# Performance work log

Measured on AMD Instinct MI355X. Metric: run time of the kernel, lower is better.

## Reference

```python
import jax, jax.numpy as jnp
import numpy as np

NUM_SPLITS = 2  # attn_splits


def _split_c_last(x, ns):
    # split_feature(channel_last=True): [b,h,w,c] -> [b*ns*ns, h/ns, w/ns, c]
    b, h, w, c = x.shape
    x = x.reshape(b, ns, h // ns, ns, w // ns, c)
    x = jnp.transpose(x, (0, 1, 3, 2, 4, 5))
    return x.reshape(b * ns * ns, h // ns, w // ns, c)


def _merge_c_last(x, ns):
    # merge_splits(channel_last=True): [b*ns*ns, hh, ww, c] -> [b, ns*hh, ns*ww, c]
    bn, hh, ww, c = x.shape
    b = bn // (ns * ns)
    x = x.reshape(b, ns, ns, hh, ww, c)
    x = jnp.transpose(x, (0, 1, 3, 2, 4, 5))
    return x.reshape(b, ns * hh, ns * ww, c)


def _make_shift_window_mask(h, w, ns):
    # exact port of generate_shift_window_attn_mask (numpy, setup-time only)
    wh, ww = h // ns, w // ns
    sh, sw = wh // 2, ww // 2
    img = np.zeros((h, w))
    cnt = 0
    for hs in (slice(0, -wh), slice(-wh, -sh), slice(-sh, None)):
        for ws in (slice(0, -ww), slice(-ww, -sw), slice(-sw, None)):
            img[hs, ws] = cnt
            cnt += 1
    mw = img.reshape(ns, wh, ns, ww).transpose(0, 2, 1, 3).reshape(ns * ns, wh * ww)
    am = mw[:, None, :] - mw[:, :, None]  # [n, i, j] = mw[n, j] - mw[n, i]
    am = np.where(am != 0, -100.0, 0.0).astype(np.float32)
    return jnp.asarray(am)


def _window_attention(q, k, v, attn_mask, h, w, ns):
    # single_head_split_window_attention with with_shift=True
    b, hw, c = q.shape
    sh, sw = (h // ns) // 2, (w // ns) // 2

    def prep(x):
        x = x.reshape(b, h, w, c)
        x = jnp.roll(x, shift=(-sh, -sw), axis=(1, 2))
        return _split_c_last(x, ns).reshape(b * ns * ns, -1, c)

    qs, ks, vs = prep(q), prep(k), prep(v)
    scale = jnp.asarray(c, q.dtype) ** 0.5
    scores = jnp.einsum('bqc,bkc->bqk', qs, ks) / scale
    scores = scores + jnp.tile(attn_mask, (b, 1, 1))
    attn = jax.nn.softmax(scores, axis=-1)
    out = jnp.einsum('bqk,bkc->bqc', attn, vs)
    out = _merge_c_last(out.reshape(b * ns * ns, h // ns, w // ns, c), ns)
    out = jnp.roll(out, shift=(sh, sw), axis=(1, 2))
    return out.reshape(b, hw, c)


def _global_correlation_softmax(feature0, feature1):
    b, c, h, w = feature0.shape
    hw = h * w
    f0 = feature0.reshape(b, c, hw).transpose(0, 2, 1)  # [b, hw, c]
    f1 = feature1.reshape(b, c, hw)                     # [b, c, hw]
    scale = jnp.asarray(c, feature0.dtype) ** 0.5
    corr = jnp.matmul(f0, f1) / scale                   # [b, hw, hw]

    yy, xx = jnp.meshgrid(jnp.arange(h), jnp.arange(w), indexing='ij')
    init_grid = jnp.stack([xx, yy], axis=0).astype(feature0.dtype)  # [2,h,w]
    init_grid = jnp.broadcast_to(init_grid[None], (b, 2, h, w))
    grid = init_grid.reshape(b, 2, hw).transpose(0, 2, 1)            # [b, hw, 2]

    corr2 = jnp.concatenate([corr, jnp.transpose(corr, (0, 2, 1))], axis=0)  # [2b,hw,hw]
    grid2 = jnp.tile(grid, (2, 1, 1))
    init2 = jnp.tile(init_grid, (2, 1, 1, 1))

    prob = jax.nn.softmax(corr2, axis=-1)
    corresp = jnp.matmul(prob, grid2).reshape(2 * b, h, w, 2)
    corresp = jnp.transpose(corresp, (0, 3, 1, 2))
    flow = corresp - init2
    f01, f10 = flow[:b], flow[b:]
    dual_prob = prob[:b] * jnp.transpose(prob[b:], (0, 2, 1))
    return f01, f10, dual_prob


def setup_inputs() -> dict:
    key = jax.random.key(0)
    b, c, h, w = 2, 128, 48, 96
    ks = jax.random.split(key, 5)
    q = jax.random.normal(ks[0], (b, h * w, c), dtype=jnp.float32)
    k = jax.random.normal(ks[1], (b, h * w, c), dtype=jnp.float32)
    v = jax.random.normal(ks[2], (b, h * w, c), dtype=jnp.float32)
    feature0 = jax.random.normal(ks[3], (b, c, h, w), dtype=jnp.float32)
    feature1 = jax.random.normal(ks[4], (b, c, h, w), dtype=jnp.float32)
    attn_mask = _make_shift_window_mask(h, w, NUM_SPLITS)
    return {"q": q, "k": k, "v": v, "feature0": feature0, "feature1": feature1,
            "attn_mask": attn_mask, "h": h, "w": w}


def reference(q, k, v, feature0, feature1, attn_mask, h, w):
    attn_out = _window_attention(q, k, v, attn_mask, h, w, NUM_SPLITS)
    f01, f10, dual_prob = _global_correlation_softmax(feature0, feature1)
    return (attn_out, f01, f10, dual_prob)
```

## Files before the change

### kernel.cpp

```cpp
#include <hip/hip_runtime.h>

#define HW 4608
#define CC 128
#define H 48
#define W 96
#define S_WIN 1152
#define SCALE 0.08838834764831845f

typedef __attribute__((ext_vector_type(8))) short bf16x8;
typedef __attribute__((ext_vector_type(4))) float f32x4;

static __device__ inline short f2bf(float f) {
    unsigned u = __builtin_bit_cast(unsigned, f);
    unsigned r = (u + 0x7fff + ((u >> 16) & 1)) >> 16;
    return (short)r;
}

__global__ __launch_bounds__(256)
void prep_all(const float* __restrict__ Q, const float* __restrict__ K, const float* __restrict__ V,
              const float* __restrict__ f0, const float* __restrict__ f1,
              bf16x8* __restrict__ cfragA, bf16x8* __restrict__ cfragB,
              bf16x8* __restrict__ qfrag, bf16x8* __restrict__ kfrag, bf16x8* __restrict__ vfrag,
              float* __restrict__ wsf)
{
    __shared__ float vt[32][132];
    const int bx = blockIdx.x;
    const int t = threadIdx.x;

    if (bx < 1152) {
        int zi = bx * 256 + t;
        if (zi < 12 * HW) wsf[zi] = 0.f;
        const int pt = bx % 72;
        const int z  = bx / 72;
        const int tensor = z >> 3, b = (z >> 2) & 1, kc = z & 3;
        const float* src = (tensor ? f1 : f0) + (size_t)b * CC * HW + (size_t)kc * 32 * HW + pt * 64;
        {
            int ch = t >> 4;
            int c4 = (t & 15) * 4;
            *(float4*)&vt[ch][c4]      = *(const float4*)&src[(size_t)ch * HW + c4];
            *(float4*)&vt[ch + 16][c4] = *(const float4*)&src[(size_t)(ch + 16) * HW + c4];
        }
        __syncthreads();
        int Rloc = t >> 6, lane = t & 63;
        int R = pt * 4 + Rloc;
        bf16x8 v;
        #pragma unroll
        for (int j = 0; j < 8; ++j) v[j] = f2bf(vt[(lane >> 4) * 8 + j][Rloc * 16 + (lane & 15)]);
        (tensor ? cfragB : cfragA)[((size_t)(b * 288 + R) * 4 + kc) * 64 + lane] = v;
    } else {
        const int bx2 = bx - 1152;
        const int R2 = bx2 % 36;
        const int z  = bx2 / 36;
        const int tensor = z >> 3, wb = z & 7;
        const int bb = wb >> 2, wi = wb & 3, si = wi >> 1, sj = wi & 1;
        const float* src = (tensor == 0 ? Q : (tensor == 1 ? K : V)) + (size_t)bb * HW * CC;
        {
            int row = t >> 3;
            int c16 = (t & 7) * 16;
            int qw = R2 * 32 + row;
            int rr = qw / 48, cc = qw - rr * 48;
            int y = (si * 24 + rr + 12) % 48;
            int x = (sj * 48 + cc + 24) % 96;
            const float* rp = src + ((size_t)y * 96 + x) * CC + c16;
            #pragma unroll
            for (int u = 0; u < 4; ++u)
                *(float4*)&vt[row][c16 + u * 4] = *(const float4*)&rp[u * 4];
        }
        __syncthreads();
        if (tensor < 2) {
            bf16x8* frag = tensor == 0 ? qfrag : kfrag;
            #pragma unroll
            for (int e2 = 0; e2 < 2; ++e2) {
                int e = t + e2 * 256;
                int Rloc = e >> 8, kc = (e >> 6) & 3, lane = e & 63;
                int R = R2 * 2 + Rloc;
                bf16x8 v;
                #pragma unroll
                for (int j = 0; j < 8; ++j)
                    v[j] = f2bf(vt[Rloc * 16 + (lane & 15)][kc * 32 + (lane >> 4) * 8 + j]);
                frag[((size_t)(wb * 72 + R) * 4 + kc) * 64 + lane] = v;
            }
        } else {
            #pragma unroll
            for (int e2 = 0; e2 < 2; ++e2) {
                int e = t + e2 * 256;
                int dB = e >> 6, lane = e & 63;
                bf16x8 v;
                #pragma unroll
                for (int j = 0; j < 8; ++j)
                    v[j] = f2bf(vt[(lane >> 4) * 8 + j][dB * 16 + (lane & 15)]);
                vfrag[((size_t)(wb * 8 + dB) * 36 + R2) * 64 + lane] = v;
            }
        }
    }
}

__global__ __launch_bounds__(256)
void fused_ws(const bf16x8* __restrict__ qfrag, const bf16x8* __restrict__ kfrag,
              const bf16x8* __restrict__ vfrag, float* __restrict__ out,
              const bf16x8* __restrict__ cfragA, const bf16x8* __restrict__ cfragB,
              float* __restrict__ rowsum, float* __restrict__ colsum)
{
    __shared__ __align__(16) char smem[38144];
    const int bx = blockIdx.x;
    const int t = threadIdx.x, lane = t & 63, w = t >> 6;

    if (bx < 576) {
        short* Psh = (short*)smem;
        unsigned char* codes = (unsigned char*)(smem + 36864);
        float* rsum_sh = (float*)(smem + 38016);
        const int qt = bx % 72, wb = bx / 72;
        const int bb = wb >> 2, wi = wb & 3, si = wi >> 1, sj = wi & 1;

        if (t < 16) rsum_sh[t] = 0.f;
        for (int i = t; i < S_WIN; i += 256) {
            int r = i / 48, c = i - r * 48;
            codes[i] = (unsigned char)((si ? (r >= 12) : 0) | ((sj ? (c >= 24) : 0) << 1));
        }
        __syncthreads();

        bf16x8 qf[4];
        {
            const bf16x8* qb = qfrag + ((size_t)(wb * 72 + qt) * 4) * 64 + lane;
            #pragma unroll
            for (int kc = 0; kc < 4; ++kc) qf[kc] = qb[kc * 64];
        }
        const int qcode = codes[qt * 16 + (lane & 15)];
        char* Pb = (char*)Psh;
        float rsum = 0.f;

        for (int kt = 0; kt < 18; ++kt) {
            int Rk = w * 18 + kt;
            const bf16x8* kb = kfrag + ((size_t)(wb * 72 + Rk) * 4) * 64 + lane;
            bf16x8 kf[4];
            #pragma unroll
            for (int kc = 0; kc < 4; ++kc) kf[kc] = kb[kc * 64];
            int k0 = Rk * 16 + (lane >> 4) * 4;
            f32x4 acc = {0.f, 0.f, 0.f, 0.f};
            #pragma unroll
            for (int kc = 0; kc < 4; ++kc)
                acc = __builtin_amdgcn_mfma_f32_16x16x32_bf16(kf[kc], qf[kc], acc, 0, 0, 0);
            float ev[4];
            #pragma unroll
            for (int r = 0; r < 4; ++r) {
                ev[r] = (codes[k0 + r] == qcode) ? __expf(acc[r] * SCALE) : 0.f;
                rsum += ev[r];
            }
            unsigned lo = (unsigned)(unsigned short)f2bf(ev[0]) | ((unsigned)(unsigned short)f2bf(ev[1]) << 16);
            unsigned hi = (unsigned)(unsigned short)f2bf(ev[2]) | ((unsigned)(unsigned short)f2bf(ev[3]) << 16);
            int qloc = lane & 15;
            int off = (qloc * 2304 + k0 * 2) ^ ((qloc & 7) << 4);
            *(uint2*)(Pb + off) = make_uint2(lo, hi);
        }
        rsum += __shfl_xor(rsum, 16); rsum += __shfl_xor(rsum, 32);
        if (lane < 16) atomicAdd(&rsum_sh[lane], rsum);
        __syncthreads();

        f32x4 pv0 = {0.f, 0.f, 0.f, 0.f}, pv1 = {0.f, 0.f, 0.f, 0.f};
        const bf16x8* vb0 = vfrag + ((size_t)(wb * 8 + w) * 36) * 64 + lane;
        const bf16x8* vb1 = vfrag + ((size_t)(wb * 8 + w + 4) * 36) * 64 + lane;
        for (int kc = 0; kc < 36; ++kc) {
            int qloc = lane & 15;
            int off = (qloc * 2304 + kc * 64 + (lane >> 4) * 16) ^ ((qloc & 7) << 4);
            bf16x8 pf = *(const bf16x8*)(Pb + off);
            pv0 = __builtin_amdgcn_mfma_f32_16x16x32_bf16(pf, vb0[kc * 64], pv0, 0, 0, 0);
            pv1 = __builtin_amdgcn_mfma_f32_16x16x32_bf16(pf, vb1[kc * 64], pv1, 0, 0, 0);
        }
        #pragma unroll
        for (int r = 0; r < 4; ++r) {
            int qloc = (lane >> 4) * 4 + r;
            float rinv = 1.f / rsum_sh[qloc];
            int qw = qt * 16 + qloc;
            int rr = qw / 48, cc2 = qw - rr * 48;
            int y = (si * 24 + rr + 12) % 48;
            int x = (sj * 48 + cc2 + 24) % 96;
            float* op = &out[((size_t)bb * HW + y * 96 + x) * CC + (lane & 15)];
            op[w * 16]       = pv0[r] * rinv;
            op[(w + 4) * 16] = pv1[r] * rinv;
        }
    } else {
        float* rs = (float*)smem;
        float* cs = (float*)(smem + 512);
        const int bx2 = bx - 576;
        const int kt = bx2 % 36, qt = (bx2 / 36) % 36, b = bx2 / 1296;
        const int wm = w >> 1, wn = w & 1;

        const bf16x8* Ab = cfragA + (size_t)(b * 288 + qt * 8 + wm * 4) * 256 + lane;
        const bf16x8* Bb = cfragB + (size_t)(b * 288 + kt * 8 + wn * 4) * 256 + lane;

        f32x4 acc[4][4] = {};
        #pragma unroll
        for (int kc = 0; kc < 4; ++kc) {
            bf16x8 a[4], bf[4];
            #pragma unroll
            for (int m = 0; m < 4; ++m) a[m]  = Ab[(m * 4 + kc) * 64];
            #pragma unroll
            for (int n = 0; n < 4; ++n) bf[n] = Bb[(n * 4 + kc) * 64];
            #pragma unroll
            for (int m = 0; m < 4; ++m)
                #pragma unroll
                for (int n = 0; n < 4; ++n)
                    acc[m][n] = __builtin_amdgcn_mfma_f32_16x16x32_bf16(a[m], bf[n], acc[m][n], 0, 0, 0);
        }

        if (t < 128) { rs[t] = 0.f; cs[t] = 0.f; }
        __syncthreads();

        float cv[4] = {};
        #pragma unroll
        for (int m = 0; m < 4; ++m) {
            float rv[4] = {};
            #pragma unroll
            for (int n = 0; n < 4; ++n)
                #pragma unroll
                for (int r = 0; r < 4; ++r) {
                    float ev = __expf(acc[m][n][r] * SCALE);
                    rv[r] += ev; cv[n] += ev;
                }
            #pragma unroll
            for (int r = 0; r < 4; ++r) {
                float s = rv[r];
                s += __shfl_xor(s, 1); s += __shfl_xor(s, 2);
                s += __shfl_xor(s, 4); s += __shfl_xor(s, 8);
                if ((lane & 15) == 0)
                    atomicAdd(&rs[wm * 64 + m * 16 + (lane >> 4) * 4 + r], s);
            }
        }
        #pragma unroll
        for (int n = 0; n < 4; ++n) {
            float s = cv[n];
            s += __shfl_xor(s, 16); s += __shfl_xor(s, 32);
            if (lane < 16) atomicAdd(&cs[wn * 64 + n * 16 + lane], s);
        }
        __syncthreads();
        if (t < 128)      atomicAdd(&rowsum[(size_t)b * HW + qt * 128 + t], rs[t]);
        else              atomicAdd(&colsum[(size_t)b * HW + kt * 128 + (t - 128)], cs[t - 128]);
    }
}

__global__ __launch_bounds__(256)
void corr_final(const bf16x8* __restrict__ fragA, const bf16x8* __restrict__ fragB,
                const float* __restrict__ rowsum, const float* __restrict__ colsum,
                float* __restrict__ rowflow, float* __restrict__ colflow,
                float* __restrict__ dual)
{
    __shared__ float sfx[128], sfy[128], scx[128], scy[128];
    __shared__ float stg[4][16][68];
    const int t = threadIdx.x, lane = t & 63, wave = t >> 6;
    const int wm = wave >> 1, wn = wave & 1;
    const int kt = blockIdx.x, qt = blockIdx.y, b = blockIdx.z;

    const bf16x8* Ab = fragA + (size_t)(b * 288 + qt * 8 + wm * 4) * 256 + lane;
    const bf16x8* Bb = fragB + (size_t)(b * 288 + kt * 8 + wn * 4) * 256 + lane;

    f32x4 acc[4][4] = {};
    #pragma unroll
    for (int kc = 0; kc < 4; ++kc) {
        bf16x8 a[4], bf[4];
        #pragma unroll
        for (int m = 0; m < 4; ++m) a[m]  = Ab[(m * 4 + kc) * 64];
        #pragma unroll
        for (int n = 0; n < 4; ++n) bf[n] = Bb[(n * 4 + kc) * 64];
        #pragma unroll
        for (int m = 0; m < 4; ++m)
            #pragma unroll
            for (int n = 0; n < 4; ++n)
                acc[m][n] = __builtin_amdgcn_mfma_f32_16x16x32_bf16(a[m], bf[n], acc[m][n], 0, 0, 0);
    }

    if (t < 128) { sfx[t] = 0.f; sfy[t] = 0.f; scx[t] = 0.f; scy[t] = 0.f; }
    __syncthreads();

    const int qbase = qt * 128 + wm * 64;
    const int kbase = kt * 128 + wn * 64;

    float cinv[4], gkx[4], gky[4];
    #pragma unroll
    for (int n = 0; n < 4; ++n) {
        int k = kbase + n * 16 + (lane & 15);
        cinv[n] = 1.f / colsum[(size_t)b * HW + k];
        int kyi = k / W;
        gkx[n] = (float)(k - kyi * W); gky[n] = (float)kyi;
    }

    float cfx[4] = {}, cfy[4] = {};
    #pragma unroll
    for (int m = 0; m < 4; ++m) {
        float rinv[4], gqx[4], gqy[4];
        int q0 = qbase + m * 16 + (lane >> 4) * 4;
        #pragma unroll
        for (int r = 0; r < 4; ++r) {
            rinv[r] = 1.f / rowsum[(size_t)b * HW + q0 + r];
            int qyi = (q0 + r) / W;
            gqx[r] = (float)(q0 + r - qyi * W); gqy[r] = (float)qyi;
        }
        float rfx[4] = {}, rfy[4] = {};
        #pragma unroll
        for (int n = 0; n < 4; ++n) {
            #pragma unroll
            for (int r = 0; r < 4; ++r) {
                float ev = __expf(acc[m][n][r] * SCALE);
                float rp = ev * rinv[r];
                float ce = ev * cinv[n];
                stg[wave][(lane >> 4) * 4 + r][n * 16 + (lane & 15)] = rp * ce;
                rfx[r] += rp * gkx[n]; rfy[r] += rp * gky[n];
                cfx[n] += ce * gqx[r]; cfy[n] += ce * gqy[r];
            }
        }
        #pragma unroll
        for (int pass = 0; pass < 4; ++pass) {
            int row = pass * 4 + (lane >> 4);
            f32x4 vv = *(const f32x4*)&stg[wave][row][(lane & 15) * 4];
            __builtin_nontemporal_store(vv,
                (f32x4*)&dual[((size_t)b * HW + qbase + m * 16 + row) * HW + kbase + (lane & 15) * 4]);
        }
        #pragma unroll
        for (int r = 0; r < 4; ++r) {
            float sx = rfx[r], sy = rfy[r];
            sx += __shfl_xor(sx, 1); sx += __shfl_xor(sx, 2);
            sx += __shfl_xor(sx, 4); sx += __shfl_xor(sx, 8);
            sy += __shfl_xor(sy, 1); sy += __shfl_xor(sy, 2);
            sy += __shfl_xor(sy, 4); sy += __shfl_xor(sy, 8);
            if ((lane & 15) == 0) {
                int row = wm * 64 + m * 16 + (lane >> 4) * 4 + r;
                atomicAdd(&sfx[row], sx); atomicAdd(&sfy[row], sy);
            }
        }
    }
    #pragma unroll
    for (int n = 0; n < 4; ++n) {
        float sx = cfx[n], sy = cfy[n];
        sx += __shfl_xor(sx, 16); sx += __shfl_xor(sx, 32);
        sy += __shfl_xor(sy, 16); sy += __shfl_xor(sy, 32);
        if (lane < 16) {
            int col = wn * 64 + n * 16 + lane;
            atomicAdd(&scx[col], sx); atomicAdd(&scy[col], sy);
        }
    }
    __syncthreads();
    if (t < 128) {
        atomicAdd(&rowflow[((size_t)b * HW + qt * 128 + t) * 2 + 0], sfx[t]);
        atomicAdd(&rowflow[((size_t)b * HW + qt * 128 + t) * 2 + 1], sfy[t]);
    } else {
        int j = t - 128;
        atomicAdd(&colflow[((size_t)b * HW + kt * 128 + j) * 2 + 0], scx[j]);
        atomicAdd(&colflow[((size_t)b * HW + kt * 128 + j) * 2 + 1], scy[j]);
    }
}

__global__ void flow_finalize(const float* __restrict__ rowflow, const float* __restrict__ colflow,
                              float* __restrict__ out)
{
    int i = blockIdx.x * 256 + threadIdx.x;
    if (i >= 2 * 2 * HW) return;
    int bb   = i / (2 * HW);
    int rem  = i % (2 * HW);
    int chan = rem / HW;
    int q    = rem % HW;
    float g = (chan == 0) ? (float)(q % W) : (float)(q / W);
    out[i]              = rowflow[((size_t)bb * HW + q) * 2 + chan] - g;
    out[2 * 2 * HW + i] = colflow[((size_t)bb * HW + q) * 2 + chan] - g;
}

extern "C" void kernel_launch(void* const* d_in, const int* in_sizes, int n_in,
                              void* d_out, int out_size, void* d_ws, size_t ws_size,
                              hipStream_t stream)
{
    (void)in_sizes; (void)n_in; (void)out_size; (void)ws_size;
    const float* q  = (const float*)d_in[0];
    const float* k  = (const float*)d_in[1];
    const float* v  = (const float*)d_in[2];
    const float* f0 = (const float*)d_in[3];
    const float* f1 = (const float*)d_in[4];

    float* out = (float*)d_out;
    const size_t ATTN_SZ = (size_t)2 * HW * CC;
    const size_t FLOW_SZ = (size_t)2 * 2 * HW;
    float* f01  = out + ATTN_SZ;
    float* dual = out + ATTN_SZ + 2 * FLOW_SZ;

    const size_t FR = 2359296;
    char* wsb = (char*)d_ws;
    bf16x8* cfragA = (bf16x8*)(wsb);
    bf16x8* cfragB = (bf16x8*)(wsb + FR);
    bf16x8* qfrag  = (bf16x8*)(wsb + 2 * FR);
    bf16x8* kfrag  = (bf16x8*)(wsb + 3 * FR);
    bf16x8* vfrag  = (bf16x8*)(wsb + 4 * FR);
    float* wsf     = (float*)(wsb + 5 * FR);
    float* rowsum  = wsf;
    float* colsum  = wsf + 2 * HW;
    float* rowflow = wsf + 4 * HW;
    float* colflow = wsf + 8 * HW;

    prep_all<<<dim3(2016), 256, 0, stream>>>(q, k, v, f0, f1, cfragA, cfragB,
                                             qfrag, kfrag, vfrag, wsf);
    fused_ws<<<dim3(576 + 2592), 256, 0, stream>>>(qfrag, kfrag, vfrag, out,
                                                   cfragA, cfragB, rowsum, colsum);
    corr_final<<<dim3(36, 36, 2), 256, 0, stream>>>(cfragA, cfragB, rowsum, colsum,
                                                    rowflow, colflow, dual);
    flow_finalize<<<dim3(72), 256, 0, stream>>>(rowflow, colflow, f01);
}
```

Before: 113.7 us.

## Split window attention P buffer into two key chunks to halve LDS

The window-attention branch now processes the 1152 keys in two chunks of 576. Each chunk writes its P tile to shared memory, then PV MFMAs consume it, which halves the P buffer and shrinks total LDS from about 38KB to about 19.7KB. The goal is more resident blocks per CU and better latency hiding. The cost is an extra barrier pair per chunk, and the correlation branch of the same kernel must now fit in the smaller shared allocation.

```diff
diff --git a/kernel.cpp b/kernel.cpp
--- a/kernel.cpp
+++ b/kernel.cpp
@@ -101,14 +101,14 @@
               const bf16x8* __restrict__ cfragA, const bf16x8* __restrict__ cfragB,
               float* __restrict__ rowsum, float* __restrict__ colsum)
 {
-    __shared__ __align__(16) char smem[38144];
+    __shared__ __align__(16) char smem[19712];
     const int bx = blockIdx.x;
     const int t = threadIdx.x, lane = t & 63, w = t >> 6;
 
     if (bx < 576) {
-        short* Psh = (short*)smem;
-        unsigned char* codes = (unsigned char*)(smem + 36864);
-        float* rsum_sh = (float*)(smem + 38016);
+        char* Pb = smem;
+        unsigned char* codes = (unsigned char*)(smem + 18432);
+        float* rsum_sh = (float*)(smem + 19584);
         const int qt = bx % 72, wb = bx / 72;
         const int bb = wb >> 2, wi = wb & 3, si = wi >> 1, sj = wi & 1;
 
@@ -126,51 +126,58 @@
             for (int kc = 0; kc < 4; ++kc) qf[kc] = qb[kc * 64];
         }
         const int qcode = codes[qt * 16 + (lane & 15)];
-        char* Pb = (char*)Psh;
+        const int qloc = lane & 15;
         float rsum = 0.f;
-
-        for (int kt = 0; kt < 18; ++kt) {
-            int Rk = w * 18 + kt;
-            const bf16x8* kb = kfrag + ((size_t)(wb * 72 + Rk) * 4) * 64 + lane;
-            bf16x8 kf[4];
-            #pragma unroll
-            for (int kc = 0; kc < 4; ++kc) kf[kc] = kb[kc * 64];
-            int k0 = Rk * 16 + (lane >> 4) * 4;
-            f32x4 acc = {0.f, 0.f, 0.f, 0.f};
-            #pragma unroll
-            for (int kc = 0; kc < 4; ++kc)
-                acc = __builtin_amdgcn_mfma_f32_16x16x32_bf16(kf[kc], qf[kc], acc, 0, 0, 0);
-            float ev[4];
-            #pragma unroll
-            for (int r = 0; r < 4; ++r) {
-                ev[r] = (codes[k0 + r] == qcode) ? __expf(acc[r] * SCALE) : 0.f;
-                rsum += ev[r];
-            }
-            unsigned lo = (unsigned)(unsigned short)f2bf(ev[0]) | ((unsigned)(unsigned short)f2bf(ev[1]) << 16);
-            unsigned hi = (unsigned)(unsigned short)f2bf(ev[2]) | ((unsigned)(unsigned short)f2bf(ev[3]) << 16);
-            int qloc = lane & 15;
-            int off = (qloc * 2304 + k0 * 2) ^ ((qloc & 7) << 4);
-            *(uint2*)(Pb + off) = make_uint2(lo, hi);
-        }
-        rsum += __shfl_xor(rsum, 16); rsum += __shfl_xor(rsum, 32);
-        if (lane < 16) atomicAdd(&rsum_sh[lane], rsum);
-        __syncthreads();
-
         f32x4 pv0 = {0.f, 0.f, 0.f, 0.f}, pv1 = {0.f, 0.f, 0.f, 0.f};
         const bf16x8* vb0 = vfrag + ((size_t)(wb * 8 + w) * 36) * 64 + lane;
         const bf16x8* vb1 = vfrag + ((size_t)(wb * 8 + w + 4) * 36) * 64 + lane;
-        for (int kc = 0; kc < 36; ++kc) {
-            int qloc = lane & 15;
-            int off = (qloc * 2304 + kc * 64 + (lane >> 4) * 16) ^ ((qloc & 7) << 4);
-            bf16x8 pf = *(const bf16x8*)(Pb + off);
-            pv0 = __builtin_amdgcn_mfma_f32_16x16x32_bf16(pf, vb0[kc * 64], pv0, 0, 0, 0);
-            pv1 = __builtin_amdgcn_mfma_f32_16x16x32_bf16(pf, vb1[kc * 64], pv1, 0, 0, 0);
+
+        #pragma unroll
+        for (int chunk = 0; chunk < 2; ++chunk) {
+            for (int kt = 0; kt < 9; ++kt) {
+                int Rk = chunk * 36 + w * 9 + kt;
+                const bf16x8* kb = kfrag + ((size_t)(wb * 72 + Rk) * 4) * 64 + lane;
+                bf16x8 kf[4];
+                #pragma unroll
+                for (int kc = 0; kc < 4; ++kc) kf[kc] = kb[kc * 64];
+                int k0 = Rk * 16 + (lane >> 4) * 4;
+                f32x4 acc = {0.f, 0.f, 0.f, 0.f};
+                #pragma unroll
+                for (int kc = 0; kc < 4; ++kc)
+                    acc = __builtin_amdgcn_mfma_f32_16x16x32_bf16(kf[kc], qf[kc], acc, 0, 0, 0);
+                float ev[4];
+                #pragma unroll
+                for (int r = 0; r < 4; ++r) {
+                    ev[r] = (codes[k0 + r] == qcode) ? __expf(acc[r] * SCALE) : 0.f;
+                    rsum += ev[r];
+                }
+                unsigned lo = (unsigned)(unsigned short)f2bf(ev[0]) | ((unsigned)(unsigned short)f2bf(ev[1]) << 16);
+                unsigned hi = (unsigned)(unsigned short)f2bf(ev[2]) | ((unsigned)(unsigned short)f2bf(ev[3]) << 16);
+                int klocal = k0 - chunk * 576;
+                int off = (qloc * 1152 + klocal * 2) ^ ((qloc & 7) << 4);
+                *(uint2*)(Pb + off) = make_uint2(lo, hi);
+            }
+            if (chunk == 1) {
+                float s = rsum;
+                s += __shfl_xor(s, 16); s += __shfl_xor(s, 32);
+                if (lane < 16) atomicAdd(&rsum_sh[lane], s);
+            }
+            __syncthreads();
+            #pragma unroll 2
+            for (int kcl = 0; kcl < 18; ++kcl) {
+                int kcg = chunk * 18 + kcl;
+                int off = (qloc * 1152 + kcl * 64 + (lane >> 4) * 16) ^ ((qloc & 7) << 4);
+                bf16x8 pf = *(const bf16x8*)(Pb + off);
+                pv0 = __builtin_amdgcn_mfma_f32_16x16x32_bf16(pf, vb0[kcg * 64], pv0, 0, 0, 0);
+                pv1 = __builtin_amdgcn_mfma_f32_16x16x32_bf16(pf, vb1[kcg * 64], pv1, 0, 0, 0);
+            }
+            __syncthreads();
         }
         #pragma unroll
         for (int r = 0; r < 4; ++r) {
-            int qloc = (lane >> 4) * 4 + r;
-            float rinv = 1.f / rsum_sh[qloc];
-            int qw = qt * 16 + qloc;
+            int ql = (lane >> 4) * 4 + r;
+            float rinv = 1.f / rsum_sh[ql];
+            int qw = qt * 16 + ql;
             int rr = qw / 48, cc2 = qw - rr * 48;
             int y = (si * 24 + rr + 12) % 48;
             int x = (sj * 48 + cc2 + 24) % 96;
```

New measurement: 126.7 us. 11.4% more time.

## Compute flow sums from unnormalized exp in first pass, fold finalize into dual kernel

Applied to the files above, without the earlier changes.

The row and column flow accumulations (exp weighted by grid coordinates) move into the first correlation pass alongside the row and column sums. Normalization by rowsum and colsum is applied later in a finalize step, so the second pass only writes the dual probability matrix. The separate finalize kernel is merged into the second pass as extra blocks, which removes one launch and the shuffle and atomic reduction work in the store-heavy pass. In exchange the first pass does more accumulation and atomics, and the finalize blocks depend on the previous kernel's results, which stream ordering already guarantees.

```diff
diff --git a/kernel.cpp b/kernel.cpp
--- a/kernel.cpp
+++ b/kernel.cpp
@@ -99,7 +99,8 @@
 void fused_ws(const bf16x8* __restrict__ qfrag, const bf16x8* __restrict__ kfrag,
               const bf16x8* __restrict__ vfrag, float* __restrict__ out,
               const bf16x8* __restrict__ cfragA, const bf16x8* __restrict__ cfragB,
-              float* __restrict__ rowsum, float* __restrict__ colsum)
+              float* __restrict__ rowsum, float* __restrict__ colsum,
+              float* __restrict__ rowflow, float* __restrict__ colflow)
 {
     __shared__ __align__(16) char smem[38144];
     const int bx = blockIdx.x;
@@ -179,8 +180,12 @@
             op[(w + 4) * 16] = pv1[r] * rinv;
         }
     } else {
-        float* rs = (float*)smem;
-        float* cs = (float*)(smem + 512);
+        float* rs   = (float*)smem;
+        float* rfxs = (float*)(smem + 512);
+        float* rfys = (float*)(smem + 1024);
+        float* cs   = (float*)(smem + 1536);
+        float* cfxs = (float*)(smem + 2048);
+        float* cfys = (float*)(smem + 2560);
         const int bx2 = bx - 576;
         const int kt = bx2 % 36, qt = (bx2 / 36) % 36, b = bx2 / 1296;
         const int wm = w >> 1, wn = w & 1;
@@ -203,52 +208,99 @@
                     acc[m][n] = __builtin_amdgcn_mfma_f32_16x16x32_bf16(a[m], bf[n], acc[m][n], 0, 0, 0);
         }
 
-        if (t < 128) { rs[t] = 0.f; cs[t] = 0.f; }
-        __syncthreads();
-
-        float cv[4] = {};
+        if (t < 128) { rs[t] = 0.f; rfxs[t] = 0.f; rfys[t] = 0.f; cs[t] = 0.f; cfxs[t] = 0.f; cfys[t] = 0.f; }
+        __syncthreads();
+
+        const int qbase = qt * 128 + wm * 64;
+        const int kbase = kt * 128 + wn * 64;
+        float gkx[4], gky[4];
+        #pragma unroll
+        for (int n = 0; n < 4; ++n) {
+            int k = kbase + n * 16 + (lane & 15);
+            int kyi = k / W;
+            gkx[n] = (float)(k - kyi * W); gky[n] = (float)kyi;
+        }
+
+        float cv[4] = {}, cfx[4] = {}, cfy[4] = {};
         #pragma unroll
         for (int m = 0; m < 4; ++m) {
-            float rv[4] = {};
+            float gqx[4], gqy[4];
+            int q0 = qbase + m * 16 + (lane >> 4) * 4;
+            #pragma unroll
+            for (int r = 0; r < 4; ++r) {
+                int qyi = (q0 + r) / W;
+                gqx[r] = (float)(q0 + r - qyi * W); gqy[r] = (float)qyi;
+            }
+            float rv[4] = {}, rfx[4] = {}, rfy[4] = {};
             #pragma unroll
             for (int n = 0; n < 4; ++n)
                 #pragma unroll
                 for (int r = 0; r < 4; ++r) {
                     float ev = __expf(acc[m][n][r] * SCALE);
-                    rv[r] += ev; cv[n] += ev;
+                    rv[r] += ev; rfx[r] += ev * gkx[n]; rfy[r] += ev * gky[n];
+                    cv[n] += ev; cfx[n] += ev * gqx[r]; cfy[n] += ev * gqy[r];
                 }
             #pragma unroll
             for (int r = 0; r < 4; ++r) {
-                float s = rv[r];
-                s += __shfl_xor(s, 1); s += __shfl_xor(s, 2);
-                s += __shfl_xor(s, 4); s += __shfl_xor(s, 8);
-                if ((lane & 15) == 0)
-                    atomicAdd(&rs[wm * 64 + m * 16 + (lane >> 4) * 4 + r], s);
+                float s0 = rv[r], s1 = rfx[r], s2 = rfy[r];
+                s0 += __shfl_xor(s0, 1); s0 += __shfl_xor(s0, 2); s0 += __shfl_xor(s0, 4); s0 += __shfl_xor(s0, 8);
+                s1 += __shfl_xor(s1, 1); s1 += __shfl_xor(s1, 2); s1 += __shfl_xor(s1, 4); s1 += __shfl_xor(s1, 8);
+                s2 += __shfl_xor(s2, 1); s2 += __shfl_xor(s2, 2); s2 += __shfl_xor(s2, 4); s2 += __shfl_xor(s2, 8);
+                if ((lane & 15) == 0) {
+                    int row = wm * 64 + m * 16 + (lane >> 4) * 4 + r;
+                    atomicAdd(&rs[row], s0); atomicAdd(&rfxs[row], s1); atomicAdd(&rfys[row], s2);
+                }
             }
         }
         #pragma unroll
         for (int n = 0; n < 4; ++n) {
-            float s = cv[n];
-            s += __shfl_xor(s, 16); s += __shfl_xor(s, 32);
-            if (lane < 16) atomicAdd(&cs[wn * 64 + n * 16 + lane], s);
-        }
-        __syncthreads();
-        if (t < 128)      atomicAdd(&rowsum[(size_t)b * HW + qt * 128 + t], rs[t]);
-        else              atomicAdd(&colsum[(size_t)b * HW + kt * 128 + (t - 128)], cs[t - 128]);
+            float s0 = cv[n], s1 = cfx[n], s2 = cfy[n];
+            s0 += __shfl_xor(s0, 16); s0 += __shfl_xor(s0, 32);
+            s1 += __shfl_xor(s1, 16); s1 += __shfl_xor(s1, 32);
+            s2 += __shfl_xor(s2, 16); s2 += __shfl_xor(s2, 32);
+            if (lane < 16) {
+                int col = wn * 64 + n * 16 + lane;
+                atomicAdd(&cs[col], s0); atomicAdd(&cfxs[col], s1); atomicAdd(&cfys[col], s2);
+            }
+        }
+        __syncthreads();
+        if (t < 128) {
+            atomicAdd(&rowsum[(size_t)b * HW + qt * 128 + t], rs[t]);
+            atomicAdd(&rowflow[((size_t)b * HW + qt * 128 + t) * 2 + 0], rfxs[t]);
+            atomicAdd(&rowflow[((size_t)b * HW + qt * 128 + t) * 2 + 1], rfys[t]);
+        } else {
+            int j = t - 128;
+            atomicAdd(&colsum[(size_t)b * HW + kt * 128 + j], cs[j]);
+            atomicAdd(&colflow[((size_t)b * HW + kt * 128 + j) * 2 + 0], cfxs[j]);
+            atomicAdd(&colflow[((size_t)b * HW + kt * 128 + j) * 2 + 1], cfys[j]);
+        }
     }
 }
 
 __global__ __launch_bounds__(256)
-void corr_final(const bf16x8* __restrict__ fragA, const bf16x8* __restrict__ fragB,
-                const float* __restrict__ rowsum, const float* __restrict__ colsum,
-                float* __restrict__ rowflow, float* __restrict__ colflow,
-                float* __restrict__ dual)
+void fused_final(const bf16x8* __restrict__ fragA, const bf16x8* __restrict__ fragB,
+                 const float* __restrict__ rowsum, const float* __restrict__ colsum,
+                 const float* __restrict__ rowflow, const float* __restrict__ colflow,
+                 float* __restrict__ dual, float* __restrict__ fout)
 {
-    __shared__ float sfx[128], sfy[128], scx[128], scy[128];
     __shared__ float stg[4][16][68];
+    const int bx = blockIdx.x;
     const int t = threadIdx.x, lane = t & 63, wave = t >> 6;
+
+    if (bx >= 2592) {
+        int i = (bx - 2592) * 256 + t;
+        int bb   = i / (2 * HW);
+        int rem  = i % (2 * HW);
+        int chan = rem / HW;
+        int q    = rem % HW;
+        float g = (chan == 0) ? (float)(q % W) : (float)(q / W);
+        fout[i]              = rowflow[((size_t)bb * HW + q) * 2 + chan] / rowsum[(size_t)bb * HW + q] - g;
+        fout[2 * 2 * HW + i] = colflow[((size_t)bb * HW + q) * 2 + chan] / colsum[(size_t)bb * HW + q] - g;
+        return;
+    }
+
+    const int kt = bx % 36, qt = (bx / 36) % 36, b = bx / 1296;
     const int wm = wave >> 1, wn = wave & 1;
-    const int kt = blockIdx.x, qt = blockIdx.y, b = blockIdx.z;
 
     const bf16x8* Ab = fragA + (size_t)(b * 288 + qt * 8 + wm * 4) * 256 + lane;
     const bf16x8* Bb = fragB + (size_t)(b * 288 + kt * 8 + wn * 4) * 256 + lane;
@@ -268,45 +320,27 @@
                 acc[m][n] = __builtin_amdgcn_mfma_f32_16x16x32_bf16(a[m], bf[n], acc[m][n], 0, 0, 0);
     }
 
-    if (t < 128) { sfx[t] = 0.f; sfy[t] = 0.f; scx[t] = 0.f; scy[t] = 0.f; }
-    __syncthreads();
-
     const int qbase = qt * 128 + wm * 64;
     const int kbase = kt * 128 + wn * 64;
 
-    float cinv[4], gkx[4], gky[4];
+    float cinv[4];
     #pragma unroll
-    for (int n = 0; n < 4; ++n) {
-        int k = kbase + n * 16 + (lane & 15);
-        cinv[n] = 1.f / colsum[(size_t)b * HW + k];
-        int kyi = k / W;
-        gkx[n] = (float)(k - kyi * W); gky[n] = (float)kyi;
-    }
-
-    float cfx[4] = {}, cfy[4] = {};
+    for (int n = 0; n < 4; ++n)
+        cinv[n] = 1.f / colsum[(size_t)b * HW + kbase + n * 16 + (lane & 15)];
+
     #pragma unroll
     for (int m = 0; m < 4; ++m) {
-        float rinv[4], gqx[4], gqy[4];
+        float rinv[4];
         int q0 = qbase + m * 16 + (lane >> 4) * 4;
         #pragma unroll
-        for (int r = 0; r < 4; ++r) {
-            rinv[r] = 1.f / rowsum[(size_t)b * HW + q0 + r];
-            int qyi = (q0 + r) / W;
-            gqx[r] = (float)(q0 + r - qyi * W); gqy[r] = (float)qyi;
-        }
-        float rfx[4] = {}, rfy[4] = {};
-        #pragma unroll
-        for (int n = 0; n < 4; ++n) {
+        for (int r = 0; r < 4; ++r) rinv[r] = 1.f / rowsum[(size_t)b * HW + q0 + r];
+        #pragma unroll
+        for (int n = 0; n < 4; ++n)
             #pragma unroll
             for (int r = 0; r < 4; ++r) {
                 float ev = __expf(acc[m][n][r] * SCALE);
-                float rp = ev * rinv[r];
-                float ce = ev * cinv[n];
-                stg[wave][(lane >> 4) * 4 + r][n * 16 + (lane & 15)] = rp * ce;
-                rfx[r] += rp * gkx[n]; rfy[r] += rp * gky[n];
-                cfx[n] += ce * gqx[r]; cfy[n] += ce * gqy[r];
-            }
-        }
+                stg[wave][(lane >> 4) * 4 + r][n * 16 + (lane & 15)] = (ev * rinv[r]) * (ev * cinv[n]);
+            }
         #pragma unroll
         for (int pass = 0; pass < 4; ++pass) {
             int row = pass * 4 + (lane >> 4);
@@ -314,52 +348,7 @@
             __builtin_nontemporal_store(vv,
                 (f32x4*)&dual[((size_t)b * HW + qbase + m * 16 + row) * HW + kbase + (lane & 15) * 4]);
         }
-        #pragma unroll
-        for (int r = 0; r < 4; ++r) {
-            float sx = rfx[r], sy = rfy[r];
-            sx += __shfl_xor(sx, 1); sx += __shfl_xor(sx, 2);
-            sx += __shfl_xor(sx, 4); sx += __shfl_xor(sx, 8);
-            sy += __shfl_xor(sy, 1); sy += __shfl_xor(sy, 2);
-            sy += __shfl_xor(sy, 4); sy += __shfl_xor(sy, 8);
-            if ((lane & 15) == 0) {
-                int row = wm * 64 + m * 16 + (lane >> 4) * 4 + r;
-                atomicAdd(&sfx[row], sx); atomicAdd(&sfy[row], sy);
-            }
-        }
-    }
-    #pragma unroll
-    for (int n = 0; n < 4; ++n) {
-        float sx = cfx[n], sy = cfy[n];
-        sx += __shfl_xor(sx, 16); sx += __shfl_xor(sx, 32);
-        sy += __shfl_xor(sy, 16); sy += __shfl_xor(sy, 32);
-        if (lane < 16) {
-            int col = wn * 64 + n * 16 + lane;
-            atomicAdd(&scx[col], sx); atomicAdd(&scy[col], sy);
-        }
-    }
-    __syncthreads();
-    if (t < 128) {
-        atomicAdd(&rowflow[((size_t)b * HW + qt * 128 + t) * 2 + 0], sfx[t]);
-        atomicAdd(&rowflow[((size_t)b * HW + qt * 128 + t) * 2 + 1], sfy[t]);
-    } else {
-        int j = t - 128;
-        atomicAdd(&colflow[((size_t)b * HW + kt * 128 + j) * 2 + 0], scx[j]);
-        atomicAdd(&colflow[((size_t)b * HW + kt * 128 + j) * 2 + 1], scy[j]);
-    }
-}
-
-__global__ void flow_finalize(const float* __restrict__ rowflow, const float* __restrict__ colflow,
-                              float* __restrict__ out)
-{
-    int i = blockIdx.x * 256 + threadIdx.x;
-    if (i >= 2 * 2 * HW) return;
-    int bb   = i / (2 * HW);
-    int rem  = i % (2 * HW);
-    int chan = rem / HW;
-    int q    = rem % HW;
-    float g = (chan == 0) ? (float)(q % W) : (float)(q / W);
-    out[i]              = rowflow[((size_t)bb * HW + q) * 2 + chan] - g;
-    out[2 * 2 * HW + i] = colflow[((size_t)bb * HW + q) * 2 + chan] - g;
+    }
 }
 
 extern "C" void kernel_launch(void* const* d_in, const int* in_sizes, int n_in,
@@ -395,8 +384,8 @@
     prep_all<<<dim3(2016), 256, 0, stream>>>(q, k, v, f0, f1, cfragA, cfragB,
                                              qfrag, kfrag, vfrag, wsf);
     fused_ws<<<dim3(576 + 2592), 256, 0, stream>>>(qfrag, kfrag, vfrag, out,
-                                                   cfragA, cfragB, rowsum, colsum);
-    corr_final<<<dim3(36, 36, 2), 256, 0, stream>>>(cfragA, cfragB, rowsum, colsum,
-                                                    rowflow, colflow, dual);
-    flow_finalize<<<dim3(72), 256, 0, stream>>>(rowflow, colflow, f01);
-}
+                                                   cfragA, cfragB, rowsum, colsum,
+                                                   rowflow, colflow);
+    fused_final<<<dim3(2592 + 72), 256, 0, stream>>>(cfragA, cfragB, rowsum, colsum,
+                                                     rowflow, colflow, dual, f01);
+}
```

New measurement: 122.8 us. +8.0%, slower.
